# Kernel tuning notes

Hardware: AMD Instinct MI355X
Metric: run time of the kernel (lower is better)

## Reference

```python
import jax, jax.numpy as jnp
import numpy as np

B, S, D = 4, 1024, 512      # batch, seq_len, input_dim (== layer_size)
M = 64                      # meta_memory_dim
L = 2                       # n_hidden_layers in ResLinear memory MLP
H = 8                       # num_attention_heads
WIN = 128                   # attention_window_size (causal sliding window)
LR, WD, MAX_ALR = 1e-3, 1e-2, 0.1
EPS = 1e-8                  # AdamW eps (betas 0.9/0.999; first step => m_hat=g, v_hat=g^2)


def lmm_fwd(lmm_W, lmm_b, x):
    # ResLinear: residual MLP, h <- h + silu(h @ W_i + b_i)
    h = x
    for i in range(L):
        h = h + jax.nn.silu(h @ lmm_W[i] + lmm_b[i])
    return h


def sliding_window_attn(x, swa_W, swa_b):
    Bsz, T, _ = x.shape
    hd = D // H
    q = (x @ swa_W[0] + swa_b[0]).reshape(Bsz, T, H, hd)
    k = (x @ swa_W[1] + swa_b[1]).reshape(Bsz, T, H, hd)
    v = (x @ swa_W[2] + swa_b[2]).reshape(Bsz, T, H, hd)
    scores = jnp.einsum('bihd,bjhd->bhij', q, k) / np.float32(np.sqrt(hd))
    i = jnp.arange(T)[:, None]
    j = jnp.arange(T)[None, :]
    mask = (j <= i) & (j > i - WIN)
    scores = jnp.where(mask, scores, jnp.float32(-1e30))
    attn = jax.nn.softmax(scores, axis=-1)
    o = jnp.einsum('bhij,bjhd->bihd', attn, v).reshape(Bsz, T, D)
    return o @ swa_W[3] + swa_b[3]


def setup_inputs() -> dict:
    key = jax.random.key(0)
    ks = jax.random.split(key, 9)
    sc = np.float32(1.0 / np.sqrt(D))
    s = lambda k, shape: jax.random.normal(k, shape, jnp.float32) * sc
    return {
        'x': jax.random.normal(ks[0], (B, S, D), jnp.float32),
        'meta_memory': jax.random.normal(ks[1], (M, D), jnp.float32),
        'lmm_W': s(ks[2], (L, D, D)),
        'lmm_b': jnp.zeros((L, D), jnp.float32),
        'Wq': s(ks[3], (D, D)), 'bq': jnp.zeros((D,), jnp.float32),
        'Wk': s(ks[4], (D, D)), 'bk': jnp.zeros((D,), jnp.float32),
        'Wv': s(ks[5], (D, D)), 'bv': jnp.zeros((D,), jnp.float32),
        'W_lr': s(ks[6], (D, 1)), 'b_lr': jnp.zeros((1,), jnp.float32),
        'swa_W': s(ks[7], (4, D, D)),  # q,k,v,out projections of SWA
        'swa_b': jnp.zeros((4, D), jnp.float32),
    }


def reference(x, meta_memory, lmm_W, lmm_b, Wq, bq, Wk, bk, Wv, bv, W_lr, b_lr, swa_W, swa_b):
    Bsz = x.shape[0]
    # inject meta memory tokens
    meta = jnp.broadcast_to(meta_memory, (Bsz, M, D))
    xm = jnp.concatenate([meta, x], axis=1)            # [B, M+S, D]

    q = xm @ Wq + bq                                   # queries  [B, T, D]
    k = xm @ Wk + bk                                   # keys
    v = xm @ Wv + bv                                   # values
    w = (jax.nn.sigmoid(xm @ W_lr + b_lr) * MAX_ALR)[..., 0]  # adaptive lr [B, T]

    # inner-loop meta-gradient of the weighted associative loss w.r.t. memory params
    def assoc_loss(params):
        preds = lmm_fwd(params[0], params[1], k)
        loss = jnp.mean((preds - v) ** 2, axis=-1)     # [B, T]
        return jnp.sum(loss * w)

    gW, gb = jax.grad(assoc_loss)((lmm_W, lmm_b))

    # one AdamW step from freshly-initialized optimizer state:
    # m_hat = g, v_hat = g^2  =>  p' = p*(1 - lr*wd) - lr * g / (|g| + eps)
    adamw = lambda p, g: p * (1.0 - LR * WD) - LR * g / (jnp.abs(g) + EPS)
    W1, b1 = adamw(lmm_W, gW), adamw(lmm_b, gb)

    # retrieval with updated memory + sliding-window attention
    retrieved = lmm_fwd(W1, b1, q)                     # [B, T, D]
    out = sliding_window_attn(retrieved, swa_W, swa_b)
    return out[:, M:, :]                               # discard meta tokens -> [B, S, D]
```

## Files before the change

### kernel.cpp

```cpp
#include <hip/hip_runtime.h>
#include <cmath>

constexpr int BB = 4, SSQ = 1024, DD = 512, MM = 64, TTK = MM + SSQ;
constexpr int HH = 8, HD = DD / HH, WINDOW = 128;
constexpr int RROWS = BB * TTK;
constexpr int OROWS = BB * SSQ;
constexpr float LR_ = 1e-3f, WD_ = 1e-2f, MAXALR_ = 0.1f, EPS_ = 1e-8f;
constexpr float C2_ = 2.0f / (float)DD;
constexpr int VPAD = 200;
constexpr int SPLITK = 17;

typedef short  s16x8 __attribute__((ext_vector_type(8)));
typedef float  f32x4 __attribute__((ext_vector_type(4)));

__device__ __forceinline__ float b2f(unsigned short u) {
    union { unsigned int i; float f; } c; c.i = ((unsigned int)u) << 16; return c.f;
}
__device__ __forceinline__ unsigned short f2b(float f) {
    union { float f; unsigned int i; } c; c.f = f;
    unsigned int r = c.i + 0x7fffu + ((c.i >> 16) & 1u);
    return (unsigned short)(r >> 16);
}
__device__ __forceinline__ float sigm(float x) { return 1.f / (1.f + __expf(-x)); }

__device__ __forceinline__ void gld16(const void* g, void* l) {
    __builtin_amdgcn_global_load_lds((const __attribute__((address_space(1))) unsigned int*)g,
                                     (__attribute__((address_space(3))) unsigned int*)l, 16, 0, 0);
}

struct GArgs {
    const unsigned short* A; const unsigned short* Bm;
    const float* bias;
    const unsigned short* aux0; const unsigned short* aux1;
    const float* wrow;
    void* out0; unsigned short* out1;
    unsigned short* outT; int tc0, tc1; float* gbOut;
    int M, N, K, lda, ld0, ld1;
};

template<int EPI, int TMM, int TNN, bool WTR, bool GBS>
__device__ __forceinline__ void mgemm_body(unsigned short* __restrict__ LB, float* __restrict__ gacc,
                                           int bx, int by, int bz, int gz, const GArgs& a, int tid)
{
    constexpr int WCOLS = TNN / 4;
    constexpr int NJ = WCOLS / 16;
    constexpr int NI = TMM / 32;
    constexpr int APASS = TMM / 64;
    constexpr int BPASS = TNN / 64;
    constexpr int ASZ = TMM * 64;
    constexpr int BSZ = TNN * 64;
    constexpr int TP  = TMM + 8;
    constexpr int CH  = TMM / 8;

    const int m0 = by * TMM, n0 = bx * TNN;
    const int ktiles = a.K >> 6;
    const int per = ktiles / gz;
    const int kt0 = bz * per, kt1 = kt0 + per;

    if (GBS && tid < 128) gacc[tid] = 0.f;

    const int r_ = tid >> 3, c_ = tid & 7;

    auto stage = [&](int buf, int kt) {
        const size_t kb = (size_t)kt * 64;
        const int sw = (c_ ^ (r_ & 7)) * 8;
#pragma unroll
        for (int p = 0; p < APASS; ++p) {
            int row = p * 64 + r_;
            gld16(a.A + (size_t)(m0 + row) * a.lda + kb + sw,
                  &LB[buf * ASZ + row * 64 + c_ * 8]);
        }
#pragma unroll
        for (int p = 0; p < BPASS; ++p) {
            int row = p * 64 + r_;
            gld16(a.Bm + (size_t)(n0 + row) * a.K + kb + sw,
                  &LB[2 * ASZ + buf * BSZ + row * 64 + c_ * 8]);
        }
    };

    f32x4 acc[NI][NJ];
#pragma unroll
    for (int i = 0; i < NI; ++i)
#pragma unroll
        for (int j = 0; j < NJ; ++j)
#pragma unroll
            for (int r = 0; r < 4; ++r) acc[i][j][r] = 0.f;

    const int lane = tid & 63, wv = tid >> 6;
    const int wr = wv & 1, wc = wv >> 1;
    const int fr = lane & 15, fg = lane >> 4;

    stage(0, kt0);
    int cur = 0;
    for (int kt = kt0; kt < kt1; ++kt) {
        __syncthreads();
        if (kt + 1 < kt1) stage(cur ^ 1, kt + 1);
#pragma unroll
        for (int ks = 0; ks < 2; ++ks) {
            s16x8 av[NI], bv[NJ];
#pragma unroll
            for (int i = 0; i < NI; ++i) {
                const int arow = wr * (TMM / 2) + i * 16 + fr;
                av[i] = *(const s16x8*)&LB[cur * ASZ + arow * 64 + (((ks * 4 + fg) ^ (arow & 7)) * 8)];
            }
#pragma unroll
            for (int j = 0; j < NJ; ++j) {
                const int brow = wc * WCOLS + j * 16 + fr;
                bv[j] = *(const s16x8*)&LB[2 * ASZ + cur * BSZ + brow * 64 + (((ks * 4 + fg) ^ (brow & 7)) * 8)];
            }
#pragma unroll
            for (int i = 0; i < NI; ++i)
#pragma unroll
                for (int j = 0; j < NJ; ++j)
                    acc[i][j] = __builtin_amdgcn_mfma_f32_16x16x32_bf16(av[i], bv[j], acc[i][j], 0, 0, 0);
        }
        cur ^= 1;
    }
    __syncthreads();

    const bool wtr_blk = WTR && (n0 >= a.tc0) && (n0 < a.tc1);
    unsigned short* TL = LB;

    float gsum[NJ];
#pragma unroll
    for (int j = 0; j < NJ; ++j) gsum[j] = 0.f;

#pragma unroll
    for (int j = 0; j < NJ; ++j) {
        const int col = n0 + wc * WCOLS + j * 16 + fr;
        const float bj = (EPI == 6 || a.bias == nullptr) ? 0.f : a.bias[col];
#pragma unroll
        for (int i = 0; i < NI; ++i) {
            const int rowb = m0 + wr * (TMM / 2) + i * 16 + fg * 4;
#pragma unroll
            for (int r = 0; r < 4; ++r) {
                const int row = rowb + r;
                const size_t off  = (size_t)row * a.N + col;
                const size_t off0 = (size_t)row * a.ld0 + col;
                const size_t off1 = (size_t)row * a.ld1 + col;
                float val = acc[i][j][r] + bj;
                float tv = val;
                if constexpr (EPI == 0) {
                    ((unsigned short*)a.out0)[off] = f2b(val);
                } else if constexpr (EPI == 1 || EPI == 2) {
                    float base = b2f(a.aux0[off0]);
                    float h = base + val * sigm(val);
                    ((unsigned short*)a.out0)[off] = f2b(h);
                    if constexpr (EPI == 2) a.out1[off] = f2b(val);
                    tv = h;
                } else if constexpr (EPI == 3) {
                    float h1 = b2f(a.aux0[off0]);
                    float pred = h1 + val * sigm(val);
                    float vv = b2f(a.aux1[off1]);
                    float d2 = C2_ * a.wrow[row] * (pred - vv);
                    float s = sigm(val);
                    float dz2 = d2 * (s * (1.f + val * (1.f - s)));
                    ((unsigned short*)a.out0)[off] = f2b(d2);
                    a.out1[off] = f2b(dz2);
                    tv = dz2;
                } else if constexpr (EPI == 4) {
                    float dh = val + b2f(a.aux0[off0]);
                    float z1 = b2f(a.aux1[off1]);
                    float s = sigm(z1);
                    float dz1v = dh * (s * (1.f + z1 * (1.f - s)));
                    ((unsigned short*)a.out0)[off] = f2b(dz1v);
                    tv = dz1v;
                } else if constexpr (EPI == 5) {
                    ((float*)a.out0)[off] = val;
                } else {
                    ((float*)a.out0)[(size_t)bz * a.ld0 + off] = val;
                }
                if (wtr_blk)
                    TL[(size_t)(col - n0) * TP + (row - m0)] = f2b(tv);
                if constexpr (GBS) gsum[j] += tv;
            }
        }
    }

    if constexpr (GBS) {
#pragma unroll
        for (int j = 0; j < NJ; ++j) {
            float s = gsum[j];
            s += __shfl_xor(s, 16);
            s += __shfl_xor(s, 32);
            if (lane < 16) atomicAdd(&gacc[wc * WCOLS + j * 16 + fr], s);
        }
    }

    if (wtr_blk || GBS) {
        __syncthreads();
        if (wtr_blk) {
            for (int idx = tid; idx < TNN * CH; idx += 512) {
                int c = idx / CH, ch = idx % CH;
                s16x8 v = *(const s16x8*)&TL[(size_t)c * TP + ch * 8];
                *(s16x8*)&a.outT[(size_t)(n0 - a.tc0 + c) * a.M + m0 + ch * 8] = v;
            }
        }
        if (GBS && tid < TNN) atomicAdd(a.gbOut + n0 + tid, gacc[tid]);
    }
}

template<int EPI, int TMM, int TNN, bool WTR, bool GBS>
__global__ __launch_bounds__(512) void mgemm(GArgs a) {
    __shared__ __align__(16) unsigned short LB[2 * TMM * 64 + 2 * TNN * 64];
    __shared__ float gacc[128];
    mgemm_body<EPI, TMM, TNN, WTR, GBS>(LB, gacc, blockIdx.x, blockIdx.y, blockIdx.z,
                                        gridDim.z, a, threadIdx.x);
}

__global__ __launch_bounds__(512) void mgemm_dual(GArgs a1, GArgs a2) {
    __shared__ __align__(16) unsigned short LB[2 * 64 * 64 + 2 * 128 * 64];
    __shared__ float gacc[128];
    int bid = blockIdx.x;
    if (bid < 544) {
        int bz = bid >> 5, rem = bid & 31;
        mgemm_body<6, 64, 128, false, false>(LB, gacc, rem & 3, rem >> 2, bz, SPLITK, a1, threadIdx.x);
    } else {
        bid -= 544;
        mgemm_body<4, 64, 64, true, true>(LB, gacc, bid & 7, bid >> 3, 0, 1, a2, threadIdx.x);
    }
}

struct TXP { const float* s[10]; unsigned short* d[10]; };
__global__ __launch_bounds__(256) void mega_setup(TXP p,
    const float* __restrict__ x, const float* __restrict__ meta, unsigned short* __restrict__ xm,
    const float* __restrict__ Wlr, const float* __restrict__ blr, float* __restrict__ w,
    const float* bq, const float* bk, const float* bv,
    const float* sb, float* cb1, float* cb2, float* gb)
{
    const int bid = blockIdx.x, tid = threadIdx.x;
    if (bid < 640) {
        __shared__ unsigned short t[64][65];
        int z = bid >> 6;
        const float* src = p.s[z];
        unsigned short* dst = p.d[z];
        int r0 = ((bid >> 3) & 7) * 64, c0 = (bid & 7) * 64;
        int lr = tid >> 4, lc = (tid & 15) * 4;
        if (z == 9) {
#pragma unroll
            for (int rr = 0; rr < 64; rr += 16) {
                size_t base = (size_t)(r0 + lr + rr) * 512 + c0 + lc;
                float4 v = *(const float4*)(src + base);
                ushort4 o; o.x = f2b(v.x); o.y = f2b(v.y); o.z = f2b(v.z); o.w = f2b(v.w);
                *(ushort4*)(dst + base) = o;
            }
            return;
        }
#pragma unroll
        for (int rr = 0; rr < 64; rr += 16) {
            float4 v = *(const float4*)(src + (size_t)(r0 + lr + rr) * 512 + c0 + lc);
            t[lr + rr][lc] = f2b(v.x); t[lr + rr][lc + 1] = f2b(v.y);
            t[lr + rr][lc + 2] = f2b(v.z); t[lr + rr][lc + 3] = f2b(v.w);
        }
        __syncthreads();
#pragma unroll
        for (int cc = 0; cc < 64; cc += 16) {
            int c = lr + cc;
            ushort4 o; o.x = t[lc][c]; o.y = t[lc + 1][c]; o.z = t[lc + 2][c]; o.w = t[lc + 3][c];
            *(ushort4*)(dst + (size_t)(c0 + c) * 512 + r0 + lc) = o;
        }
        return;
    }
    if (bid < 640 + RROWS) {
        __shared__ float sm[4];
        int row = bid - 640;
        int b = row / TTK, tt = row % TTK;
        const float* src = (tt < MM) ? meta + (size_t)tt * DD
                                     : x + ((size_t)b * SSQ + (tt - MM)) * DD;
        float x0 = src[tid], x1 = src[tid + 256];
        unsigned short* dst = xm + (size_t)row * DD;
        dst[tid] = f2b(x0); dst[tid + 256] = f2b(x1);
        float s = x0 * Wlr[tid] + x1 * Wlr[tid + 256];
        for (int o2 = 32; o2; o2 >>= 1) s += __shfl_down(s, o2);
        if ((tid & 63) == 0) sm[tid >> 6] = s;
        __syncthreads();
        if (tid == 0) w[row] = MAXALR_ / (1.f + __expf(-(sm[0] + sm[1] + sm[2] + sm[3] + blr[0])));
        return;
    }
    int i = (bid - 640 - RROWS) * 256 + tid;
    if (i < 1536) {
        float v = (i < 512) ? bq[i] : (i < 1024) ? bk[i - 512] : bv[i - 1024];
        cb1[i] = v; cb2[i] = sb[i];
    } else if (i < 2560) {
        gb[i - 1536] = 0.f;
    }
}

__global__ __launch_bounds__(256) void adamw_transp(const float* __restrict__ W,
                                                    const float* __restrict__ gWp,
                                                    unsigned short* __restrict__ dstBase,
                                                    const float* __restrict__ pb,
                                                    const float* __restrict__ gB,
                                                    float* __restrict__ bnOut) {
    if (blockIdx.z == 2) {
        int idx = (blockIdx.y * 8 + blockIdx.x) * 256 + threadIdx.x;
        if (idx < 2 * DD) {
            float gg = gB[idx];
            bnOut[idx] = pb[idx] * (1.f - LR_ * WD_) - LR_ * gg / (fabsf(gg) + EPS_);
        }
        return;
    }
    const int m = blockIdx.z;
    const float* src = W + (size_t)m * DD * DD;
    unsigned short* dst = dstBase + (size_t)m * DD * DD;
    __shared__ unsigned short t[64][65];
    int r0 = blockIdx.y * 64, c0 = blockIdx.x * 64;
    int lr = threadIdx.x >> 4, lc = (threadIdx.x & 15) * 4;
#pragma unroll
    for (int rr = 0; rr < 64; rr += 16) {
        size_t base = (size_t)(r0 + lr + rr) * 512 + c0 + lc;
        float4 v = *(const float4*)(src + base);
        float gx = 0.f, gy = 0.f, gz = 0.f, gw = 0.f;
        for (int z = 0; z < SPLITK; ++z) {
            const float4 p4 = *(const float4*)(gWp + ((size_t)z * 2 + m) * DD * DD + base);
            gx += p4.x; gy += p4.y; gz += p4.z; gw += p4.w;
        }
        t[lr + rr][lc]     = f2b(v.x * (1.f - LR_ * WD_) - LR_ * gx / (fabsf(gx) + EPS_));
        t[lr + rr][lc + 1] = f2b(v.y * (1.f - LR_ * WD_) - LR_ * gy / (fabsf(gy) + EPS_));
        t[lr + rr][lc + 2] = f2b(v.z * (1.f - LR_ * WD_) - LR_ * gz / (fabsf(gz) + EPS_));
        t[lr + rr][lc + 3] = f2b(v.w * (1.f - LR_ * WD_) - LR_ * gw / (fabsf(gw) + EPS_));
    }
    __syncthreads();
#pragma unroll
    for (int cc = 0; cc < 64; cc += 16) {
        int c = lr + cc;
        ushort4 o; o.x = t[lc][c]; o.y = t[lc + 1][c]; o.z = t[lc + 2][c]; o.w = t[lc + 3][c];
        *(ushort4*)(dst + (size_t)(c0 + c) * 512 + r0 + lc) = o;
    }
}

__global__ __launch_bounds__(256) void swa_mfma(const unsigned short* __restrict__ AQ,
                                                unsigned short* __restrict__ O) {
    __shared__ unsigned short Qs[64 * 64];
    __shared__ unsigned short KP[192 * 64];
    __shared__ unsigned short Vt[64 * VPAD];

    const int tid = threadIdx.x;
    const int qt = blockIdx.x, h = blockIdx.y, b = blockIdx.z;
    const int i0 = MM + qt * 64;
    const int jbase = i0 - 128;
    const int r_ = tid >> 3, c_ = tid & 7;

#pragma unroll
    for (int rd = 0; rd < 2; ++rd) {
        int r = rd * 32 + r_;
        const unsigned short* src = AQ + ((size_t)(b * TTK + i0 + r)) * 1536 + h * HD
                                    + ((c_ ^ (r & 7)) * 8);
        gld16(src, &Qs[rd * 2048 + tid * 8]);
    }
#pragma unroll
    for (int rd = 0; rd < 6; ++rd) {
        int r = rd * 32 + r_;
        int j = jbase + r; if (j < 0) j = 0;
        const unsigned short* src = AQ + ((size_t)(b * TTK + j)) * 1536 + 512 + h * HD
                                    + ((c_ ^ (r & 7)) * 8);
        gld16(src, &KP[rd * 2048 + tid * 8]);
    }
#pragma unroll
    for (int rd = 0; rd < 6; ++rd) {
        int r = rd * 32 + r_;
        int j = jbase + r; if (j < 0) j = 0;
        const s16x8 vv = *(const s16x8*)(AQ + ((size_t)(b * TTK + j)) * 1536 + 1024 + h * HD + c_ * 8);
#pragma unroll
        for (int i = 0; i < 8; ++i)
            Vt[(c_ * 8 + i) * VPAD + r] = (unsigned short)vv[i];
    }
    __syncthreads();

    const int lane = tid & 63, w = tid >> 6;
    const int g = lane >> 4, fl = lane & 15;
    const int qA = w * 16 + fl;
    const int swzA = qA & 7;

    f32x4 sc[12];
#pragma unroll
    for (int t = 0; t < 12; ++t) { sc[t][0] = 0.f; sc[t][1] = 0.f; sc[t][2] = 0.f; sc[t][3] = 0.f; }

#pragma unroll
    for (int ks = 0; ks < 2; ++ks) {
        s16x8 af = *(const s16x8*)&Qs[qA * 64 + (((4 * ks + g) ^ swzA) * 8)];
#pragma unroll
        for (int t = 0; t < 12; ++t) {
            int jn = t * 16 + fl;
            s16x8 bf = *(const s16x8*)&KP[jn * 64 + (((4 * ks + g) ^ (jn & 7)) * 8)];
            sc[t] = __builtin_amdgcn_mfma_f32_16x16x32_bf16(af, bf, sc[t], 0, 0, 0);
        }
    }

    const int kmin = (i0 < 128) ? (128 - i0) : 0;
    float mx[4] = {-1e30f, -1e30f, -1e30f, -1e30f};
#pragma unroll
    for (int t = 0; t < 12; ++t) {
        int kk = t * 16 + fl;
#pragma unroll
        for (int r = 0; r < 4; ++r) {
            int qb = w * 16 + g * 4 + r;
            bool m = (kk > qb) && (kk <= qb + 128) && (kk >= kmin);
            float v = m ? sc[t][r] * 0.125f : -1e30f;
            sc[t][r] = v;
            mx[r] = fmaxf(mx[r], v);
        }
    }
#pragma unroll
    for (int r = 0; r < 4; ++r) {
        mx[r] = fmaxf(mx[r], __shfl_xor(mx[r], 1));
        mx[r] = fmaxf(mx[r], __shfl_xor(mx[r], 2));
        mx[r] = fmaxf(mx[r], __shfl_xor(mx[r], 4));
        mx[r] = fmaxf(mx[r], __shfl_xor(mx[r], 8));
    }
    float ls[4] = {0.f, 0.f, 0.f, 0.f};
#pragma unroll
    for (int t = 0; t < 12; ++t) {
#pragma unroll
        for (int r = 0; r < 4; ++r) {
            float p = __expf(sc[t][r] - mx[r]);
            sc[t][r] = p;
            ls[r] += p;
        }
    }
#pragma unroll
    for (int r = 0; r < 4; ++r) {
        ls[r] += __shfl_xor(ls[r], 1);
        ls[r] += __shfl_xor(ls[r], 2);
        ls[r] += __shfl_xor(ls[r], 4);
        ls[r] += __shfl_xor(ls[r], 8);
    }

    __syncthreads();

#pragma unroll
    for (int t = 0; t < 12; ++t) {
        int kk = t * 16 + fl;
#pragma unroll
        for (int r = 0; r < 4; ++r) {
            int qb = w * 16 + g * 4 + r;
            int ch = (kk >> 3) ^ (qb & 7);
            KP[qb * 192 + ch * 8 + (kk & 7)] = f2b(sc[t][r]);
        }
    }
    __syncthreads();

    f32x4 oacc[4];
#pragma unroll
    for (int dt = 0; dt < 4; ++dt) { oacc[dt][0] = 0.f; oacc[dt][1] = 0.f; oacc[dt][2] = 0.f; oacc[dt][3] = 0.f; }
#pragma unroll
    for (int js = 0; js < 6; ++js) {
        s16x8 pa = *(const s16x8*)&KP[qA * 192 + (((js * 4 + g) ^ swzA) * 8)];
#pragma unroll
        for (int dt = 0; dt < 4; ++dt) {
            s16x8 bv = *(const s16x8*)&Vt[(dt * 16 + fl) * VPAD + js * 32 + g * 8];
            oacc[dt] = __builtin_amdgcn_mfma_f32_16x16x32_bf16(pa, bv, oacc[dt], 0, 0, 0);
        }
    }

    float inv[4];
#pragma unroll
    for (int r = 0; r < 4; ++r) inv[r] = 1.f / ls[r];
#pragma unroll
    for (int dt = 0; dt < 4; ++dt) {
#pragma unroll
        for (int r = 0; r < 4; ++r) {
            int qb = w * 16 + g * 4 + r;
            int srow = qt * 64 + qb;
            int d = dt * 16 + fl;
            O[((size_t)b * SSQ + srow) * DD + h * HD + d] = f2b(oacc[dt][r] * inv[r]);
        }
    }
}

extern "C" void kernel_launch(void* const* d_in, const int* in_sizes, int n_in,
                              void* d_out, int out_size, void* d_ws, size_t ws_size,
                              hipStream_t stream) {
    const float* x    = (const float*)d_in[0];
    const float* meta = (const float*)d_in[1];
    const float* lmmW = (const float*)d_in[2];
    const float* lmmb = (const float*)d_in[3];
    const float* Wq   = (const float*)d_in[4];
    const float* bq   = (const float*)d_in[5];
    const float* Wk   = (const float*)d_in[6];
    const float* bk   = (const float*)d_in[7];
    const float* Wv   = (const float*)d_in[8];
    const float* bv   = (const float*)d_in[9];
    const float* Wlr  = (const float*)d_in[10];
    const float* blr  = (const float*)d_in[11];
    const float* swaW = (const float*)d_in[12];
    const float* swab = (const float*)d_in[13];
    float* out = (float*)d_out;
    (void)in_sizes; (void)n_in; (void)out_size; (void)ws_size;

    char* wsb = (char*)d_ws;
    size_t off = 0;
    auto alloc = [&](size_t bytes) -> void* {
        void* p = wsb + off; off = (off + bytes + 255) & ~(size_t)255; return p;
    };
    const size_t BIGE = (size_t)RROWS * DD;
    unsigned short* qkv  = (unsigned short*)alloc((size_t)RROWS * 1536 * 2);
    unsigned short* xm   = (unsigned short*)alloc(BIGE * 2);
    unsigned short* h1   = (unsigned short*)alloc(BIGE * 2);
    unsigned short* z1   = (unsigned short*)alloc(BIGE * 2);
    unsigned short* d2   = (unsigned short*)alloc(BIGE * 2);
    unsigned short* dz2  = (unsigned short*)alloc(BIGE * 2);
    unsigned short* dz1  = (unsigned short*)alloc(BIGE * 2);
    unsigned short* h1r  = (unsigned short*)alloc(BIGE * 2);
    unsigned short* retr = (unsigned short*)alloc(BIGE * 2);
    unsigned short* o    = (unsigned short*)alloc((size_t)OROWS * DD * 2);
    unsigned short* kT   = (unsigned short*)alloc(BIGE * 2);
    unsigned short* h1T  = (unsigned short*)alloc(BIGE * 2);
    unsigned short* dz2T = (unsigned short*)alloc(BIGE * 2);
    unsigned short* dz1T = (unsigned short*)alloc(BIGE * 2);
    unsigned short* Wt   = (unsigned short*)alloc((size_t)12 * DD * DD * 2);
    float* gWp  = (float*)alloc((size_t)SPLITK * 2 * DD * DD * 4);
    float* w    = (float*)alloc((size_t)RROWS * 4);
    float* gb   = (float*)alloc(1024 * 4);
    float* bn   = (float*)alloc(1024 * 4);
    float* cbQ  = (float*)alloc(1536 * 4);
    float* cbS  = (float*)alloc(1536 * 4);
    auto WT = [&](int i) { return Wt + (size_t)i * DD * DD; };

    TXP tp{};
    tp.s[0] = Wq;             tp.d[0] = WT(0);
    tp.s[1] = Wk;             tp.d[1] = WT(1);
    tp.s[2] = Wv;             tp.d[2] = WT(2);
    tp.s[3] = lmmW;           tp.d[3] = WT(3);
    tp.s[4] = lmmW + DD * DD; tp.d[4] = WT(4);
    tp.s[5] = swaW + 0 * DD * DD; tp.d[5] = WT(5);
    tp.s[6] = swaW + 1 * DD * DD; tp.d[6] = WT(6);
    tp.s[7] = swaW + 2 * DD * DD; tp.d[7] = WT(7);
    tp.s[8] = swaW + 3 * DD * DD; tp.d[8] = WT(8);
    tp.s[9] = lmmW + DD * DD; tp.d[9] = WT(9);
    mega_setup<<<640 + RROWS + 10, 256, 0, stream>>>(tp, x, meta, xm, Wlr, blr, w,
                                                     bq, bk, bv, swab, cbQ, cbS, gb);

    auto ga = [](const unsigned short* A, const unsigned short* Bm, const float* bias,
                 const unsigned short* a0, const unsigned short* a1, const float* wr,
                 void* o0, unsigned short* o1, unsigned short* oT, int t0, int t1, float* gbo,
                 int M, int N, int K, int lda, int l0, int l1) {
        GArgs g{A, Bm, bias, a0, a1, wr, o0, o1, oT, t0, t1, gbo, M, N, K, lda, l0, l1};
        return g;
    };
    const dim3 gB(512);

    mgemm<0, 64, 128, true, false><<<dim3(12, 68), gB, 0, stream>>>(
        ga(xm, WT(0), cbQ, nullptr, nullptr, nullptr, qkv, nullptr, kT, 512, 1024, nullptr,
           RROWS, 1536, DD, DD, 0, 0));

    mgemm<2, 64, 64, true, false><<<dim3(8, 68), gB, 0, stream>>>(
        ga(qkv + 512, WT(3), lmmb, qkv + 512, nullptr, nullptr, h1, z1, h1T, 0, 512, nullptr,
           RROWS, DD, DD, 1536, 1536, 0));
    mgemm<3, 64, 64, true, true><<<dim3(8, 68), gB, 0, stream>>>(
        ga(h1, WT(4), lmmb + DD, h1, qkv + 1024, w, d2, dz2, dz2T, 0, 512, gb + DD,
           RROWS, DD, DD, DD, DD, 1536));

    mgemm_dual<<<1088, gB, 0, stream>>>(
        ga(h1T, dz2T, nullptr, nullptr, nullptr, nullptr, gWp + DD * DD, nullptr, nullptr, 0, 0, nullptr,
           DD, DD, RROWS, RROWS, 2 * DD * DD, 0),
        ga(dz2, WT(9), nullptr, d2, z1, nullptr, dz1, nullptr, dz1T, 0, 512, gb,
           RROWS, DD, DD, DD, DD, DD));

    mgemm<6, 64, 128, false, false><<<dim3(4, 8, SPLITK), gB, 0, stream>>>(
        ga(kT, dz1T, nullptr, nullptr, nullptr, nullptr, gWp, nullptr, nullptr, 0, 0, nullptr,
           DD, DD, RROWS, RROWS, 2 * DD * DD, 0));

    adamw_transp<<<dim3(8, 8, 3), 256, 0, stream>>>(lmmW, gWp, WT(10), lmmb, gb, bn);

    mgemm<1, 64, 64, false, false><<<dim3(8, 68), gB, 0, stream>>>(
        ga(qkv, WT(10), bn, qkv, nullptr, nullptr, h1r, nullptr, nullptr, 0, 0, nullptr,
           RROWS, DD, DD, 1536, 1536, 0));
    mgemm<1, 64, 64, false, false><<<dim3(8, 68), gB, 0, stream>>>(
        ga(h1r, WT(11), bn + DD, h1r, nullptr, nullptr, retr, nullptr, nullptr, 0, 0, nullptr,
           RROWS, DD, DD, DD, DD, 0));

    mgemm<0, 64, 128, false, false><<<dim3(12, 68), gB, 0, stream>>>(
        ga(retr, WT(5), cbS, nullptr, nullptr, nullptr, qkv, nullptr, nullptr, 0, 0, nullptr,
           RROWS, 1536, DD, DD, 0, 0));
    swa_mfma<<<dim3(16, 8, 4), 256, 0, stream>>>(qkv, o);
    mgemm<5, 64, 64, false, false><<<dim3(8, 64), gB, 0, stream>>>(
        ga(o, WT(8), swab + 3 * DD, nullptr, nullptr, nullptr, out, nullptr, nullptr, 0, 0, nullptr,
           OROWS, DD, DD, DD, 0, 0));
}
```

Baseline: 224.9 us.

## Use fixed 64x64 tiles with triple-buffered LDS pipeline and explicit vmcnt waits

Removes the tile-size template parameters so every GEMM uses a 64x64 tile. The mainloop becomes a three-stage LDS ring with loads issued two k-tiles ahead, explicit s_waitcnt vmcnt and a raw barrier in place of __syncthreads. Grids for the 1536-wide QKV GEMMs and the split-K weight-gradient GEMMs are doubled to match. This aims to hide global-load latency and add more blocks for better CU occupancy, at the cost of less register reuse per wave (two MFMAs per k-step) and more A-tile reloads.

```diff
diff --git a/kernel.cpp b/kernel.cpp
--- a/kernel.cpp
+++ b/kernel.cpp
@@ -38,24 +38,19 @@
     int M, N, K, lda, ld0, ld1;
 };
 
-template<int EPI, int TMM, int TNN, bool WTR, bool GBS>
+constexpr int ASZ = 64 * 64;
+constexpr int LBSZ = 6 * ASZ;
+
+template<int EPI, bool WTR, bool GBS>
 __device__ __forceinline__ void mgemm_body(unsigned short* __restrict__ LB, float* __restrict__ gacc,
                                            int bx, int by, int bz, int gz, const GArgs& a, int tid)
 {
-    constexpr int WCOLS = TNN / 4;
-    constexpr int NJ = WCOLS / 16;
-    constexpr int NI = TMM / 32;
-    constexpr int APASS = TMM / 64;
-    constexpr int BPASS = TNN / 64;
-    constexpr int ASZ = TMM * 64;
-    constexpr int BSZ = TNN * 64;
-    constexpr int TP  = TMM + 8;
-    constexpr int CH  = TMM / 8;
-
-    const int m0 = by * TMM, n0 = bx * TNN;
+    constexpr int TP = 72;
+    const int m0 = by * 64, n0 = bx * 64;
     const int ktiles = a.K >> 6;
     const int per = ktiles / gz;
-    const int kt0 = bz * per, kt1 = kt0 + per;
+    const int kt0 = bz * per;
+    const int nt = per;
 
     if (GBS && tid < 128) gacc[tid] = 0.f;
 
@@ -64,81 +59,63 @@
     auto stage = [&](int buf, int kt) {
         const size_t kb = (size_t)kt * 64;
         const int sw = (c_ ^ (r_ & 7)) * 8;
-#pragma unroll
-        for (int p = 0; p < APASS; ++p) {
-            int row = p * 64 + r_;
-            gld16(a.A + (size_t)(m0 + row) * a.lda + kb + sw,
-                  &LB[buf * ASZ + row * 64 + c_ * 8]);
-        }
-#pragma unroll
-        for (int p = 0; p < BPASS; ++p) {
-            int row = p * 64 + r_;
-            gld16(a.Bm + (size_t)(n0 + row) * a.K + kb + sw,
-                  &LB[2 * ASZ + buf * BSZ + row * 64 + c_ * 8]);
-        }
+        gld16(a.A + (size_t)(m0 + r_) * a.lda + kb + sw,
+              &LB[buf * 2 * ASZ + r_ * 64 + c_ * 8]);
+        gld16(a.Bm + (size_t)(n0 + r_) * a.K + kb + sw,
+              &LB[buf * 2 * ASZ + ASZ + r_ * 64 + c_ * 8]);
     };
 
-    f32x4 acc[NI][NJ];
-#pragma unroll
-    for (int i = 0; i < NI; ++i)
-#pragma unroll
-        for (int j = 0; j < NJ; ++j)
-#pragma unroll
-            for (int r = 0; r < 4; ++r) acc[i][j][r] = 0.f;
+    f32x4 acc[2];
+    acc[0][0] = 0.f; acc[0][1] = 0.f; acc[0][2] = 0.f; acc[0][3] = 0.f;
+    acc[1] = acc[0];
 
     const int lane = tid & 63, wv = tid >> 6;
     const int wr = wv & 1, wc = wv >> 1;
     const int fr = lane & 15, fg = lane >> 4;
 
     stage(0, kt0);
-    int cur = 0;
-    for (int kt = kt0; kt < kt1; ++kt) {
-        __syncthreads();
-        if (kt + 1 < kt1) stage(cur ^ 1, kt + 1);
+    if (nt > 1) stage(1, kt0 + 1);
+    for (int it = 0; it < nt; ++it) {
+        if (it + 1 < nt) asm volatile("s_waitcnt vmcnt(2)" ::: "memory");
+        else             asm volatile("s_waitcnt vmcnt(0)" ::: "memory");
+        __builtin_amdgcn_s_barrier();
+        if (it + 2 < nt) stage((it + 2) % 3, kt0 + it + 2);
+        const int cb = (it % 3) * 2 * ASZ;
 #pragma unroll
         for (int ks = 0; ks < 2; ++ks) {
-            s16x8 av[NI], bv[NJ];
-#pragma unroll
-            for (int i = 0; i < NI; ++i) {
-                const int arow = wr * (TMM / 2) + i * 16 + fr;
-                av[i] = *(const s16x8*)&LB[cur * ASZ + arow * 64 + (((ks * 4 + fg) ^ (arow & 7)) * 8)];
+            s16x8 av[2], bv;
+#pragma unroll
+            for (int i = 0; i < 2; ++i) {
+                const int arow = wr * 32 + i * 16 + fr;
+                av[i] = *(const s16x8*)&LB[cb + arow * 64 + (((ks * 4 + fg) ^ (arow & 7)) * 8)];
             }
-#pragma unroll
-            for (int j = 0; j < NJ; ++j) {
-                const int brow = wc * WCOLS + j * 16 + fr;
-                bv[j] = *(const s16x8*)&LB[2 * ASZ + cur * BSZ + brow * 64 + (((ks * 4 + fg) ^ (brow & 7)) * 8)];
-            }
-#pragma unroll
-            for (int i = 0; i < NI; ++i)
-#pragma unroll
-                for (int j = 0; j < NJ; ++j)
-                    acc[i][j] = __builtin_amdgcn_mfma_f32_16x16x32_bf16(av[i], bv[j], acc[i][j], 0, 0, 0);
-        }
-        cur ^= 1;
+            const int brow = wc * 16 + fr;
+            bv = *(const s16x8*)&LB[cb + ASZ + brow * 64 + (((ks * 4 + fg) ^ (brow & 7)) * 8)];
+#pragma unroll
+            for (int i = 0; i < 2; ++i)
+                acc[i] = __builtin_amdgcn_mfma_f32_16x16x32_bf16(av[i], bv, acc[i], 0, 0, 0);
+        }
     }
     __syncthreads();
 
     const bool wtr_blk = WTR && (n0 >= a.tc0) && (n0 < a.tc1);
     unsigned short* TL = LB;
 
-    float gsum[NJ];
-#pragma unroll
-    for (int j = 0; j < NJ; ++j) gsum[j] = 0.f;
-
-#pragma unroll
-    for (int j = 0; j < NJ; ++j) {
-        const int col = n0 + wc * WCOLS + j * 16 + fr;
+    float gsum = 0.f;
+
+    {
+        const int col = n0 + wc * 16 + fr;
         const float bj = (EPI == 6 || a.bias == nullptr) ? 0.f : a.bias[col];
 #pragma unroll
-        for (int i = 0; i < NI; ++i) {
-            const int rowb = m0 + wr * (TMM / 2) + i * 16 + fg * 4;
+        for (int i = 0; i < 2; ++i) {
+            const int rowb = m0 + wr * 32 + i * 16 + fg * 4;
 #pragma unroll
             for (int r = 0; r < 4; ++r) {
                 const int row = rowb + r;
                 const size_t off  = (size_t)row * a.N + col;
                 const size_t off0 = (size_t)row * a.ld0 + col;
                 const size_t off1 = (size_t)row * a.ld1 + col;
-                float val = acc[i][j][r] + bj;
+                float val = acc[i][r] + bj;
                 float tv = val;
                 if constexpr (EPI == 0) {
                     ((unsigned short*)a.out0)[off] = f2b(val);
@@ -172,52 +149,49 @@
                 }
                 if (wtr_blk)
                     TL[(size_t)(col - n0) * TP + (row - m0)] = f2b(tv);
-                if constexpr (GBS) gsum[j] += tv;
+                if constexpr (GBS) gsum += tv;
             }
         }
     }
 
     if constexpr (GBS) {
-#pragma unroll
-        for (int j = 0; j < NJ; ++j) {
-            float s = gsum[j];
-            s += __shfl_xor(s, 16);
-            s += __shfl_xor(s, 32);
-            if (lane < 16) atomicAdd(&gacc[wc * WCOLS + j * 16 + fr], s);
-        }
+        float s = gsum;
+        s += __shfl_xor(s, 16);
+        s += __shfl_xor(s, 32);
+        if (lane < 16) atomicAdd(&gacc[wc * 16 + fr], s);
     }
 
     if (wtr_blk || GBS) {
         __syncthreads();
         if (wtr_blk) {
-            for (int idx = tid; idx < TNN * CH; idx += 512) {
-                int c = idx / CH, ch = idx % CH;
+            for (int idx = tid; idx < 64 * 8; idx += 512) {
+                int c = idx >> 3, ch = idx & 7;
                 s16x8 v = *(const s16x8*)&TL[(size_t)c * TP + ch * 8];
                 *(s16x8*)&a.outT[(size_t)(n0 - a.tc0 + c) * a.M + m0 + ch * 8] = v;
             }
         }
-        if (GBS && tid < TNN) atomicAdd(a.gbOut + n0 + tid, gacc[tid]);
-    }
-}
-
-template<int EPI, int TMM, int TNN, bool WTR, bool GBS>
+        if (GBS && tid < 64) atomicAdd(a.gbOut + n0 + tid, gacc[tid]);
+    }
+}
+
+template<int EPI, bool WTR, bool GBS>
 __global__ __launch_bounds__(512) void mgemm(GArgs a) {
-    __shared__ __align__(16) unsigned short LB[2 * TMM * 64 + 2 * TNN * 64];
+    __shared__ __align__(16) unsigned short LB[LBSZ];
     __shared__ float gacc[128];
-    mgemm_body<EPI, TMM, TNN, WTR, GBS>(LB, gacc, blockIdx.x, blockIdx.y, blockIdx.z,
-                                        gridDim.z, a, threadIdx.x);
+    mgemm_body<EPI, WTR, GBS>(LB, gacc, blockIdx.x, blockIdx.y, blockIdx.z,
+                              gridDim.z, a, threadIdx.x);
 }
 
 __global__ __launch_bounds__(512) void mgemm_dual(GArgs a1, GArgs a2) {
-    __shared__ __align__(16) unsigned short LB[2 * 64 * 64 + 2 * 128 * 64];
+    __shared__ __align__(16) unsigned short LB[LBSZ];
     __shared__ float gacc[128];
     int bid = blockIdx.x;
-    if (bid < 544) {
-        int bz = bid >> 5, rem = bid & 31;
-        mgemm_body<6, 64, 128, false, false>(LB, gacc, rem & 3, rem >> 2, bz, SPLITK, a1, threadIdx.x);
+    if (bid < 1088) {
+        int bz = bid >> 6, rem = bid & 63;
+        mgemm_body<6, false, false>(LB, gacc, rem & 7, rem >> 3, bz, SPLITK, a1, threadIdx.x);
     } else {
-        bid -= 544;
-        mgemm_body<4, 64, 64, true, true>(LB, gacc, bid & 7, bid >> 3, 0, 1, a2, threadIdx.x);
+        bid -= 1088;
+        mgemm_body<4, true, true>(LB, gacc, bid & 7, bid >> 3, 0, 1, a2, threadIdx.x);
     }
 }
 
@@ -540,41 +514,41 @@
     };
     const dim3 gB(512);
 
-    mgemm<0, 64, 128, true, false><<<dim3(12, 68), gB, 0, stream>>>(
+    mgemm<0, true, false><<<dim3(24, 68), gB, 0, stream>>>(
         ga(xm, WT(0), cbQ, nullptr, nullptr, nullptr, qkv, nullptr, kT, 512, 1024, nullptr,
            RROWS, 1536, DD, DD, 0, 0));
 
-    mgemm<2, 64, 64, true, false><<<dim3(8, 68), gB, 0, stream>>>(
+    mgemm<2, true, false><<<dim3(8, 68), gB, 0, stream>>>(
         ga(qkv + 512, WT(3), lmmb, qkv + 512, nullptr, nullptr, h1, z1, h1T, 0, 512, nullptr,
            RROWS, DD, DD, 1536, 1536, 0));
-    mgemm<3, 64, 64, true, true><<<dim3(8, 68), gB, 0, stream>>>(
+    mgemm<3, true, true><<<dim3(8, 68), gB, 0, stream>>>(
         ga(h1, WT(4), lmmb + DD, h1, qkv + 1024, w, d2, dz2, dz2T, 0, 512, gb + DD,
            RROWS, DD, DD, DD, DD, 1536));
 
-    mgemm_dual<<<1088, gB, 0, stream>>>(
+    mgemm_dual<<<1632, gB, 0, stream>>>(
         ga(h1T, dz2T, nullptr, nullptr, nullptr, nullptr, gWp + DD * DD, nullptr, nullptr, 0, 0, nullptr,
            DD, DD, RROWS, RROWS, 2 * DD * DD, 0),
         ga(dz2, WT(9), nullptr, d2, z1, nullptr, dz1, nullptr, dz1T, 0, 512, gb,
            RROWS, DD, DD, DD, DD, DD));
 
-    mgemm<6, 64, 128, false, false><<<dim3(4, 8, SPLITK), gB, 0, stream>>>(
+    mgemm<6, false, false><<<dim3(8, 8, SPLITK), gB, 0, stream>>>(
         ga(kT, dz1T, nullptr, nullptr, nullptr, nullptr, gWp, nullptr, nullptr, 0, 0, nullptr,
            DD, DD, RROWS, RROWS, 2 * DD * DD, 0));
 
     adamw_transp<<<dim3(8, 8, 3), 256, 0, stream>>>(lmmW, gWp, WT(10), lmmb, gb, bn);
 
-    mgemm<1, 64, 64, false, false><<<dim3(8, 68), gB, 0, stream>>>(
+    mgemm<1, false, false><<<dim3(8, 68), gB, 0, stream>>>(
         ga(qkv, WT(10), bn, qkv, nullptr, nullptr, h1r, nullptr, nullptr, 0, 0, nullptr,
            RROWS, DD, DD, 1536, 1536, 0));
-    mgemm<1, 64, 64, false, false><<<dim3(8, 68), gB, 0, stream>>>(
+    mgemm<1, false, false><<<dim3(8, 68), gB, 0, stream>>>(
         ga(h1r, WT(11), bn + DD, h1r, nullptr, nullptr, retr, nullptr, nullptr, 0, 0, nullptr,
            RROWS, DD, DD, DD, DD, 0));
 
-    mgemm<0, 64, 128, false, false><<<dim3(12, 68), gB, 0, stream>>>(
+    mgemm<0, false, false><<<dim3(24, 68), gB, 0, stream>>>(
         ga(retr, WT(5), cbS, nullptr, nullptr, nullptr, qkv, nullptr, nullptr, 0, 0, nullptr,
            RROWS, 1536, DD, DD, 0, 0));
     swa_mfma<<<dim3(16, 8, 4), 256, 0, stream>>>(qkv, o);
-    mgemm<5, 64, 64, false, false><<<dim3(8, 64), gB, 0, stream>>>(
+    mgemm<5, false, false><<<dim3(8, 64), gB, 0, stream>>>(
         ga(o, WT(8), swab + 3 * DD, nullptr, nullptr, nullptr, out, nullptr, nullptr, 0, 0, nullptr,
            OROWS, DD, DD, DD, 0, 0));
 }
```

New measurement: 235.6 us. +4.7%, slower.
